# Kernel optimization log

Measured on AMD Instinct MI355X. Metric: run time of the kernel, lower is better.

Reference implementation:

```python
import jax, jax.numpy as jnp
import numpy as np

F = 512    # x_features
M = 8      # mid_features
C = 20     # classnum
B = 2048   # batch
MF = M * F

def _lin(k, fin, fout):
    k1, k2 = jax.random.split(k)
    s = 1.0 / np.sqrt(fin)
    W = jax.random.uniform(k1, (fout, fin), minval=-s, maxval=s, dtype=jnp.float32)
    b = jax.random.uniform(k2, (fout,), minval=-s, maxval=s, dtype=jnp.float32)
    return W, b

def setup_inputs():
    key = jax.random.key(0)
    ks = jax.random.split(key, 12)
    W1, b1 = _lin(ks[0], F, F)
    W2, b2 = _lin(ks[1], F, F)
    W3, b3 = _lin(ks[2], F, MF)
    W4, b4 = _lin(ks[3], F, MF)
    W5, b5 = _lin(ks[4], MF, C)
    W7, b7 = _lin(ks[5], MF, MF)
    W8, b8 = _lin(ks[6], MF, MF)
    W9, b9 = _lin(ks[7], MF, MF)
    x = jax.random.normal(ks[8], (B, F), dtype=jnp.float32)
    batch_label = jax.random.randint(ks[9], (B,), 0, C, dtype=jnp.int32)
    hs_init = jax.random.uniform(ks[10], (C, MF), dtype=jnp.float32)
    labels_init = jnp.zeros((C, MF), dtype=jnp.float32)
    return dict(x=x, batch_label=batch_label, W1=W1, b1=b1, W2=W2, b2=b2,
                W3=W3, b3=b3, W4=W4, b4=b4, W5=W5, b5=b5, W7=W7, b7=b7,
                W8=W8, b8=b8, W9=W9, b9=b9, hs_init=hs_init, labels_init=labels_init)

def reference(x, batch_label, W1, b1, W2, b2, W3, b3, W4, b4, W5, b5,
              W7, b7, W8, b8, W9, b9, hs_init, labels_init):
    h = jax.nn.relu(x @ W1.T + b1)
    h = jax.nn.relu(h @ W2.T + b2)
    label0 = jnp.tanh(h @ W3.T + b3)   # [B, MF]  (self.label_0)
    out = jnp.tanh(h @ W4.T + b4)      # [B, MF]
    gram = label0 @ label0.T           # [B, B]
    masks = batch_label[None, :] == jnp.arange(C, dtype=batch_label.dtype)[:, None]  # [C, B]
    counts = masks.sum(axis=1)         # [C]

    def attn_for_class(mask):
        # masked self-attention restricted to rows/cols of this class
        logits = jnp.where(mask[None, :], gram, -1e30)
        A = jax.nn.softmax(logits, axis=1)           # [B, B]
        attn = A @ label0                            # [B, MF]
        return jnp.sum(attn * mask[:, None].astype(attn.dtype), axis=0) / jnp.maximum(mask.sum(), 1)

    attn_labels = jax.vmap(attn_for_class)(masks)    # [C, MF]
    hs_new = jax.nn.sigmoid(attn_labels @ W7.T + b7 + hs_init @ W8.T + b8)
    hs_new = jax.lax.stop_gradient(hs_new)           # matches hs[i].detach_()
    nonempty = (counts > 0)[:, None]
    hs = jnp.where(nonempty, hs_new, hs_init)
    labels = jnp.where(nonempty, jnp.tanh(hs @ W9.T + b9), labels_init)  # [C, MF]
    # cosine similarity (torch eps = 1e-8)
    denom = jnp.maximum(jnp.linalg.norm(out, axis=1)[:, None] *
                        jnp.linalg.norm(labels, axis=1)[None, :], 1e-8)
    outs = (out @ labels.T) / denom                  # [B, C]  == outs.transpose(1,0)
    ls = jnp.tanh(labels @ W5.T + b5)                # [C, C]
    return jnp.concatenate([outs, ls], axis=0)       # [B+C, C]
```

## Files before the change

kernel.cpp:

```cpp
#include <hip/hip_runtime.h>
#include <hip/hip_bf16.h>
#include <math.h>

#define FDIM 512
#define MFD  4096
#define CNUM 20
#define BATCH 2048
#define SMAX 256
#define GKS  16
#define GBK  64
#define SKS  4
#define AJS  4

typedef __attribute__((ext_vector_type(8))) short bf16x8;
typedef __attribute__((ext_vector_type(4))) float f32x4;

__device__ inline unsigned short f2bf1(float f) {
  union { float f; unsigned u; } a; a.f = f;
  unsigned r = a.u + 0x7fffu + ((a.u >> 16) & 1u);
  return (unsigned short)(r >> 16);
}
__device__ inline float bf2f(unsigned short u) {
  union { unsigned u; float f; } a; a.u = ((unsigned)u) << 16; return a.f;
}
__device__ inline float fast_tanh(float x) {
  float cx = fminf(fmaxf(x, -15.f), 15.f);
  float e = __expf(2.f * cx);
  return (e - 1.f) / (e + 1.f);
}
__device__ inline float dot4acc(float4 a, float4 b, float acc) {
  acc = fmaf(a.x, b.x, acc); acc = fmaf(a.y, b.y, acc);
  acc = fmaf(a.z, b.z, acc); acc = fmaf(a.w, b.w, acc);
  return acc;
}
__device__ inline void gload_lds16(const void* g, void* l) {
  __builtin_amdgcn_global_load_lds(
      (const __attribute__((address_space(1))) unsigned int*)g,
      (__attribute__((address_space(3))) unsigned int*)l, 16, 0, 0);
}

__global__ __launch_bounds__(256) void cvt_bf16(const float* __restrict__ in,
                                                unsigned short* __restrict__ out, int n4) {
  int i = blockIdx.x * 256 + threadIdx.x;
  if (i >= n4) return;
  float4 v = ((const float4*)in)[i];
  ((ushort4*)out)[i] = make_ushort4(f2bf1(v.x), f2bf1(v.y), f2bf1(v.z), f2bf1(v.w));
}

template<int ACT, int OUTBF>
__global__ __launch_bounds__(256) void mfma_gemm(const unsigned short* __restrict__ A,
                                                 const unsigned short* __restrict__ B,
                                                 const float* __restrict__ bias,
                                                 float* __restrict__ Cf,
                                                 unsigned short* __restrict__ Cb,
                                                 int M, int N, int K) {
  __shared__ __align__(16) char lds[16384];
  const int t = threadIdx.x, lane = t & 63, w = t >> 6;
  const int wr = w >> 1, wc = w & 1;
  const int m0 = blockIdx.y * 128, n0 = blockIdx.x * 128;

  f32x4 acc[4][4];
#pragma unroll
  for (int m = 0; m < 4; ++m)
#pragma unroll
    for (int n = 0; n < 4; ++n) acc[m][n] = (f32x4){0.f, 0.f, 0.f, 0.f};

  int rS[2], qS[2];
#pragma unroll
  for (int i = 0; i < 2; ++i) {
    int t16 = (w * 2 + i) * 64 + lane;
    rS[i] = t16 >> 2;
    qS[i] = (t16 & 3) ^ ((rS[i] >> 1) & 3);
  }

  for (int k0 = 0; k0 < K; k0 += 32) {
#pragma unroll
    for (int i = 0; i < 2; ++i) {
      gload_lds16(A + (size_t)(m0 + rS[i]) * K + k0 + qS[i] * 8,
                  lds + (w * 2 + i) * 1024);
      gload_lds16(B + (size_t)(n0 + rS[i]) * K + k0 + qS[i] * 8,
                  lds + 8192 + (w * 2 + i) * 1024);
    }
    __syncthreads();

    bf16x8 af[4], bfr[4];
    const int kq = lane >> 4, l15 = lane & 15;
#pragma unroll
    for (int m = 0; m < 4; ++m) {
      int ra = wr * 64 + m * 16 + l15;
      af[m] = *(const bf16x8*)(lds + ra * 64 + ((kq ^ ((ra >> 1) & 3)) << 4));
      int rb = wc * 64 + m * 16 + l15;
      bfr[m] = *(const bf16x8*)(lds + 8192 + rb * 64 + ((kq ^ ((rb >> 1) & 3)) << 4));
    }
#pragma unroll
    for (int m = 0; m < 4; ++m)
#pragma unroll
      for (int n = 0; n < 4; ++n)
        acc[m][n] = __builtin_amdgcn_mfma_f32_16x16x32_bf16(af[m], bfr[n], acc[m][n], 0, 0, 0);
    __syncthreads();
  }

#pragma unroll
  for (int n = 0; n < 4; ++n) {
    int col = n0 + wc * 64 + n * 16 + (lane & 15);
    float bv = bias[col];
#pragma unroll
    for (int m = 0; m < 4; ++m) {
      int rbase = m0 + wr * 64 + m * 16 + ((lane >> 4) << 2);
#pragma unroll
      for (int j = 0; j < 4; ++j) {
        float v = acc[m][n][j] + bv;
        if (ACT == 1) v = fmaxf(v, 0.f);
        if (ACT == 2) v = fast_tanh(v);
        if (OUTBF) Cb[(size_t)(rbase + j) * N + col] = f2bf1(v);
        else       Cf[(size_t)(rbase + j) * N + col] = v;
      }
    }
  }
}

__global__ void build_idx(const int* __restrict__ label, int* __restrict__ idx,
                          int* __restrict__ counts) {
  __shared__ int cnt[CNUM];
  int t = threadIdx.x;
  if (t < CNUM) cnt[t] = 0;
  __syncthreads();
  for (int b = t; b < BATCH; b += 256) {
    int c = label[b];
    int p = atomicAdd(&cnt[c], 1);
    idx[c * BATCH + p] = b;
  }
  __syncthreads();
  if (t < CNUM) counts[t] = cnt[t];
}

__global__ __launch_bounds__(256) void gram_mfma(const unsigned short* __restrict__ Gb,
                                                 const int* __restrict__ idx,
                                                 const int* __restrict__ counts,
                                                 float* __restrict__ S) {
  const int c = blockIdx.z, n = counts[c];
  const int tp = blockIdx.y, ti = tp >> 1, tj = tp & 1;
  const int i0 = ti * 128, j0 = tj * 128;
  if (i0 >= n || j0 >= n) return;
  const int* idc = idx + c * BATCH;
  __shared__ __align__(16) char lds[32768];
  const bool same = (ti == tj);
  char* ldsB = same ? lds : (lds + 16384);

  const int t = threadIdx.x, lane = t & 63, w = t >> 6;
  size_t offA[4], offB[4];
#pragma unroll
  for (int q = 0; q < 4; ++q) {
    int t16 = q * 256 + t;
    int r = t16 >> 3, p = t16 & 7;
    int ch = p ^ (r & 7);
    int ia = i0 + r, jb = j0 + r;
    offA[q] = (size_t)idc[ia < n ? ia : 0] * MFD + ch * 8;
    offB[q] = (size_t)idc[jb < n ? jb : 0] * MFD + ch * 8;
  }
  const int kbeg = blockIdx.x * (MFD / GKS);

  f32x4 acc[2][8];
#pragma unroll
  for (int fi = 0; fi < 2; ++fi)
#pragma unroll
    for (int fj = 0; fj < 8; ++fj) acc[fi][fj] = (f32x4){0.f, 0.f, 0.f, 0.f};

  const int l15 = lane & 15, kq = lane >> 4;
  for (int k0 = kbeg; k0 < kbeg + MFD / GKS; k0 += GBK) {
#pragma unroll
    for (int q = 0; q < 4; ++q) {
      gload_lds16(Gb + offA[q] + k0, lds + q * 4096 + w * 1024 + (lane << 4));
      if (!same)
        gload_lds16(Gb + offB[q] + k0, ldsB + q * 4096 + w * 1024 + (lane << 4));
    }
    __syncthreads();
#pragma unroll
    for (int kk = 0; kk < 2; ++kk) {
      bf16x8 a[2], b[8];
#pragma unroll
      for (int fi = 0; fi < 2; ++fi) {
        int r = w * 32 + fi * 16 + l15;
        int sl = (kk * 4 + kq) ^ (r & 7);
        a[fi] = *(const bf16x8*)(lds + r * 128 + sl * 16);
      }
#pragma unroll
      for (int fj = 0; fj < 8; ++fj) {
        int r = fj * 16 + l15;
        int sl = (kk * 4 + kq) ^ (r & 7);
        b[fj] = *(const bf16x8*)(ldsB + r * 128 + sl * 16);
      }
#pragma unroll
      for (int fi = 0; fi < 2; ++fi)
#pragma unroll
        for (int fj = 0; fj < 8; ++fj)
          acc[fi][fj] = __builtin_amdgcn_mfma_f32_16x16x32_bf16(a[fi], b[fj], acc[fi][fj], 0, 0, 0);
    }
    __syncthreads();
  }

  float* Sc = S + (size_t)c * SMAX * SMAX;
#pragma unroll
  for (int fi = 0; fi < 2; ++fi) {
    int ibase = i0 + w * 32 + fi * 16 + (lane >> 4) * 4;
#pragma unroll
    for (int fj = 0; fj < 8; ++fj) {
      int j = j0 + fj * 16 + l15;
#pragma unroll
      for (int jj = 0; jj < 4; ++jj)
        atomicAdd(&Sc[(size_t)(ibase + jj) * SMAX + j], acc[fi][fj][jj]);
    }
  }
}

__global__ __launch_bounds__(256) void softmax_w2(const float* __restrict__ S,
                                                  const int* __restrict__ counts,
                                                  float* __restrict__ W) {
  const int c = blockIdx.y;
  const int n = counts[c];
  __shared__ float wacc[4][SMAX];
  const int t = threadIdx.x, lane = t & 63, wid = t >> 6;
  for (int j = t; j < 4 * SMAX; j += 256) (&wacc[0][0])[j] = 0.f;
  __syncthreads();
  const float* Sc = S + (size_t)c * SMAX * SMAX;
  for (int i = blockIdx.x * 4 + wid; i < n; i += 32) {
    const float* row = Sc + (size_t)i * SMAX;
    float v[4];
    float m = -INFINITY;
#pragma unroll
    for (int q = 0; q < 4; ++q) {
      int j = lane + q * 64;
      v[q] = (j < n) ? row[j] : -INFINITY;
      m = fmaxf(m, v[q]);
    }
#pragma unroll
    for (int s = 32; s; s >>= 1) m = fmaxf(m, __shfl_xor(m, s));
    float e[4], sum = 0.f;
#pragma unroll
    for (int q = 0; q < 4; ++q) {
      int j = lane + q * 64;
      e[q] = (j < n) ? expf(v[q] - m) : 0.f;
      sum += e[q];
    }
#pragma unroll
    for (int s = 32; s; s >>= 1) sum += __shfl_xor(sum, s);
    float inv = 1.f / sum;
#pragma unroll
    for (int q = 0; q < 4; ++q) {
      int j = lane + q * 64;
      if (j < n) wacc[wid][j] += e[q] * inv;
    }
  }
  __syncthreads();
  for (int j = t; j < SMAX; j += 256) {
    float v = wacc[0][j] + wacc[1][j] + wacc[2][j] + wacc[3][j];
    if (v != 0.f) atomicAdd(&W[c * SMAX + j], v);
  }
}

__global__ __launch_bounds__(256) void attn_combine3(const unsigned short* __restrict__ Gb,
                                                     const int* __restrict__ idx,
                                                     const int* __restrict__ counts,
                                                     const float* __restrict__ W,
                                                     float* __restrict__ attn) {
  const int c = blockIdx.z, n = counts[c];
  const int col2 = blockIdx.x * 256 + threadIdx.x;
  const int j0 = (n * (int)blockIdx.y) / AJS;
  const int j1 = (n * ((int)blockIdx.y + 1)) / AJS;
  const int* idc = idx + c * BATCH;
  const float* Wc = W + c * SMAX;
  float a0 = 0.f, a1 = 0.f;
  for (int j = j0; j < j1; ++j) {
    float wj = Wc[j];
    ushort2 g = ((const ushort2*)(Gb + (size_t)idc[j] * MFD))[col2];
    a0 = fmaf(wj, bf2f(g.x), a0);
    a1 = fmaf(wj, bf2f(g.y), a1);
  }
  if (j1 > j0) {
    float inv = 1.f / (float)n;
    atomicAdd(&attn[(size_t)c * MFD + col2 * 2],     a0 * inv);
    atomicAdd(&attn[(size_t)c * MFD + col2 * 2 + 1], a1 * inv);
  }
}

template<int TWO>
__global__ __launch_bounds__(256) void skinny_acc(const float* __restrict__ Wa,
                                                  const float* __restrict__ Aa,
                                                  const float* __restrict__ Wb,
                                                  const float* __restrict__ Ab,
                                                  float* __restrict__ accbuf) {
  const int t = threadIdx.x, lane = t & 63, wid = t >> 6;
  const int o = blockIdx.x * 4 + wid;
  const int kb4 = blockIdx.y * (MFD / 4 / SKS);
  const float4* W4a = (const float4*)Wa + (size_t)o * (MFD / 4) + kb4;
  const float4* W4b = (const float4*)Wb + (size_t)o * (MFD / 4) + kb4;
  const float4* A4a = (const float4*)Aa + kb4;
  const float4* A4b = (const float4*)Ab + kb4;
  float acc[CNUM] = {};
#pragma unroll
  for (int i = 0; i < MFD / 4 / SKS / 64; ++i) {
    int k4 = i * 64 + lane;
    float4 wv = W4a[k4];
    float4 wv2;
    if (TWO) wv2 = W4b[k4];
#pragma unroll
    for (int c = 0; c < CNUM; ++c) {
      acc[c] = dot4acc(A4a[(size_t)c * (MFD / 4) + k4], wv, acc[c]);
      if (TWO) acc[c] = dot4acc(A4b[(size_t)c * (MFD / 4) + k4], wv2, acc[c]);
    }
  }
#pragma unroll
  for (int c = 0; c < CNUM; ++c)
#pragma unroll
    for (int s = 32; s; s >>= 1) acc[c] += __shfl_xor(acc[c], s);
#pragma unroll
  for (int c = 0; c < CNUM; ++c)
    if (lane == c) atomicAdd(&accbuf[(size_t)o * CNUM + c], acc[c]);
}

__global__ __launch_bounds__(256) void finalize_hs(const float* __restrict__ accbuf,
                                                   const float* __restrict__ b7,
                                                   const float* __restrict__ b8,
                                                   const int* __restrict__ counts,
                                                   const float* __restrict__ hsin,
                                                   float* __restrict__ hs) {
  const int o = blockIdx.x * 256 + threadIdx.x;
  const float bb = b7[o] + b8[o];
#pragma unroll
  for (int c = 0; c < CNUM; ++c) {
    float v = accbuf[(size_t)o * CNUM + c] + bb;
    v = 1.f / (1.f + __expf(-v));
    hs[(size_t)c * MFD + o] = (counts[c] > 0) ? v : hsin[(size_t)c * MFD + o];
  }
}

__global__ __launch_bounds__(256) void finalize_lab(const float* __restrict__ accbuf,
                                                    const float* __restrict__ b9,
                                                    const int* __restrict__ counts,
                                                    const float* __restrict__ labinit,
                                                    float* __restrict__ labels) {
  const int o = blockIdx.x * 256 + threadIdx.x;
  const float bb = b9[o];
#pragma unroll
  for (int c = 0; c < CNUM; ++c) {
    float v = tanhf(accbuf[(size_t)o * CNUM + c] + bb);
    labels[(size_t)c * MFD + o] = (counts[c] > 0) ? v : labinit[(size_t)c * MFD + o];
  }
}

__global__ __launch_bounds__(256) void rownorm(const float* __restrict__ X,
                                               float* __restrict__ out, int ncols) {
  const int b = blockIdx.x, t = threadIdx.x;
  const float4* X4 = (const float4*)(X + (size_t)b * ncols);
  float ss = 0.f;
  for (int i = t; i < ncols / 4; i += 256) {
    float4 v = X4[i];
    ss = dot4acc(v, v, ss);
  }
#pragma unroll
  for (int s = 32; s; s >>= 1) ss += __shfl_xor(ss, s);
  __shared__ float red[4];
  const int lane = t & 63, wid = t >> 6;
  if (lane == 0) red[wid] = ss;
  __syncthreads();
  if (t == 0) out[b] = sqrtf(red[0] + red[1] + red[2] + red[3]);
}

__global__ __launch_bounds__(256) void outs_fused(const float* __restrict__ outb,
                                                  const float* __restrict__ labels,
                                                  const float* __restrict__ nl,
                                                  float* __restrict__ dout) {
  const int b = blockIdx.x, t = threadIdx.x;
  const float4* O4 = (const float4*)(outb + (size_t)b * MFD);
  const float4* L4 = (const float4*)labels;
  float acc[CNUM] = {};
  float ss = 0.f;
  for (int i = t; i < MFD / 4; i += 256) {
    float4 ov = O4[i];
    ss = dot4acc(ov, ov, ss);
#pragma unroll
    for (int c = 0; c < CNUM; ++c)
      acc[c] = dot4acc(ov, L4[(size_t)c * (MFD / 4) + i], acc[c]);
  }
#pragma unroll
  for (int s = 32; s; s >>= 1) ss += __shfl_xor(ss, s);
#pragma unroll
  for (int c = 0; c < CNUM; ++c)
#pragma unroll
    for (int s = 32; s; s >>= 1) acc[c] += __shfl_xor(acc[c], s);
  __shared__ float red[4][CNUM + 1];
  const int lane = t & 63, wid = t >> 6;
  if (lane == 0) {
#pragma unroll
    for (int c = 0; c < CNUM; ++c) red[wid][c] = acc[c];
    red[wid][CNUM] = ss;
  }
  __syncthreads();
  if (t < CNUM) {
    float v = red[0][t] + red[1][t] + red[2][t] + red[3][t];
    float nrm = sqrtf(red[0][CNUM] + red[1][CNUM] + red[2][CNUM] + red[3][CNUM]);
    float d = fmaxf(nrm * nl[t], 1e-8f);
    dout[(size_t)b * CNUM + t] = v / d;
  }
}

__global__ __launch_bounds__(256) void ls_kernel(const float* __restrict__ labels,
                                                 const float* __restrict__ W5,
                                                 const float* __restrict__ b5,
                                                 float* __restrict__ dout) {
  const int c1 = blockIdx.x, t = threadIdx.x;
  __shared__ float lrow[MFD];
  for (int i = t; i < MFD; i += 256) lrow[i] = labels[(size_t)c1 * MFD + i];
  __syncthreads();
  const int lane = t & 63, wid = t >> 6;
  for (int c2 = wid; c2 < CNUM; c2 += 4) {
    const float4* w = (const float4*)(W5 + (size_t)c2 * MFD);
    float acc = 0.f;
    for (int i = lane; i < MFD / 4; i += 64)
      acc = dot4acc(*(const float4*)&lrow[i * 4], w[i], acc);
#pragma unroll
    for (int s = 32; s; s >>= 1) acc += __shfl_xor(acc, s);
    if (lane == 0)
      dout[(size_t)(BATCH + c1) * CNUM + c2] = tanhf(acc + b5[c2]);
  }
}

extern "C" void kernel_launch(void* const* d_in, const int* in_sizes, int n_in,
                              void* d_out, int out_size, void* d_ws, size_t ws_size,
                              hipStream_t stream) {
  const float* x    = (const float*)d_in[0];
  const int*   lab  = (const int*)d_in[1];
  const float* W1 = (const float*)d_in[2];  const float* b1 = (const float*)d_in[3];
  const float* W2 = (const float*)d_in[4];  const float* b2 = (const float*)d_in[5];
  const float* W3 = (const float*)d_in[6];  const float* b3 = (const float*)d_in[7];
  const float* W4 = (const float*)d_in[8];  const float* b4 = (const float*)d_in[9];
  const float* W5 = (const float*)d_in[10]; const float* b5 = (const float*)d_in[11];
  const float* W7 = (const float*)d_in[12]; const float* b7 = (const float*)d_in[13];
  const float* W8 = (const float*)d_in[14]; const float* b8 = (const float*)d_in[15];
  const float* W9 = (const float*)d_in[16]; const float* b9 = (const float*)d_in[17];
  const float* hs_init  = (const float*)d_in[18];
  const float* lab_init = (const float*)d_in[19];
  float* out = (float*)d_out;

  char* base = (char*)d_ws;
  size_t off = 0;
  auto alloc = [&](size_t bytes) { char* p = base + off; off += (bytes + 255) & ~(size_t)255; return p; };

  unsigned short* xb  = (unsigned short*)alloc((size_t)BATCH * FDIM * 2);
  unsigned short* h1b = (unsigned short*)alloc((size_t)BATCH * FDIM * 2);
  unsigned short* h2b = (unsigned short*)alloc((size_t)BATCH * FDIM * 2);
  unsigned short* W1b = (unsigned short*)alloc((size_t)FDIM * FDIM * 2);
  unsigned short* W2b = (unsigned short*)alloc((size_t)FDIM * FDIM * 2);
  unsigned short* W3b = (unsigned short*)alloc((size_t)MFD * FDIM * 2);
  unsigned short* W4b = (unsigned short*)alloc((size_t)MFD * FDIM * 2);
  unsigned short* label0b = (unsigned short*)alloc((size_t)BATCH * MFD * 2);
  float* outb   = (float*)alloc((size_t)BATCH * MFD * 4);
  float* S      = (float*)alloc((size_t)CNUM * SMAX * SMAX * 4);
  float* wsum   = (float*)alloc((size_t)CNUM * SMAX * 4);
  float* attn   = (float*)alloc((size_t)CNUM * MFD * 4);
  float* accA   = (float*)alloc((size_t)MFD * CNUM * 4);
  float* accB   = (float*)alloc((size_t)MFD * CNUM * 4);
  float* hsbuf  = (float*)alloc((size_t)CNUM * MFD * 4);
  float* labels = (float*)alloc((size_t)CNUM * MFD * 4);
  float* nl     = (float*)alloc(64 * 4);
  int* idx      = (int*)alloc((size_t)CNUM * BATCH * 4);
  int* counts   = (int*)alloc(64 * 4);

  cvt_bf16<<<(BATCH * FDIM / 4 + 255) / 256, 256, 0, stream>>>(x,  xb,  BATCH * FDIM / 4);
  cvt_bf16<<<(FDIM * FDIM / 4 + 255) / 256, 256, 0, stream>>>(W1, W1b, FDIM * FDIM / 4);
  cvt_bf16<<<(FDIM * FDIM / 4 + 255) / 256, 256, 0, stream>>>(W2, W2b, FDIM * FDIM / 4);
  cvt_bf16<<<(MFD * FDIM / 4 + 255) / 256, 256, 0, stream>>>(W3, W3b, MFD * FDIM / 4);
  cvt_bf16<<<(MFD * FDIM / 4 + 255) / 256, 256, 0, stream>>>(W4, W4b, MFD * FDIM / 4);

  mfma_gemm<1, 1><<<dim3(FDIM / 128, BATCH / 128), 256, 0, stream>>>(xb,  W1b, b1, nullptr, h1b, BATCH, FDIM, FDIM);
  mfma_gemm<1, 1><<<dim3(FDIM / 128, BATCH / 128), 256, 0, stream>>>(h1b, W2b, b2, nullptr, h2b, BATCH, FDIM, FDIM);
  mfma_gemm<2, 1><<<dim3(MFD / 128, BATCH / 128), 256, 0, stream>>>(h2b, W3b, b3, nullptr, label0b, BATCH, MFD, FDIM);
  mfma_gemm<2, 0><<<dim3(MFD / 128, BATCH / 128), 256, 0, stream>>>(h2b, W4b, b4, outb,   nullptr,  BATCH, MFD, FDIM);

  build_idx<<<1, 256, 0, stream>>>(lab, idx, counts);
  hipMemsetAsync(S, 0, (size_t)CNUM * SMAX * SMAX * 4 + (size_t)CNUM * SMAX * 4 + (size_t)CNUM * MFD * 4, stream);
  hipMemsetAsync(accA, 0, (size_t)MFD * CNUM * 8, stream);
  gram_mfma<<<dim3(GKS, 4, CNUM), 256, 0, stream>>>(label0b, idx, counts, S);
  softmax_w2<<<dim3(8, CNUM), 256, 0, stream>>>(S, counts, wsum);
  attn_combine3<<<dim3(MFD / 512, AJS, CNUM), 256, 0, stream>>>(label0b, idx, counts, wsum, attn);

  skinny_acc<1><<<dim3(MFD / 4, SKS), 256, 0, stream>>>(W7, attn, W8, hs_init, accA);
  finalize_hs<<<MFD / 256, 256, 0, stream>>>(accA, b7, b8, counts, hs_init, hsbuf);
  skinny_acc<0><<<dim3(MFD / 4, SKS), 256, 0, stream>>>(W9, hsbuf, nullptr, nullptr, accB);
  finalize_lab<<<MFD / 256, 256, 0, stream>>>(accB, b9, counts, lab_init, labels);

  rownorm<<<CNUM, 256, 0, stream>>>(labels, nl, MFD);
  outs_fused<<<BATCH, 256, 0, stream>>>(outb, labels, nl, out);
  ls_kernel<<<CNUM, 256, 0, stream>>>(labels, W5, b5, out);
}
```

Measured before the change: 627.3 us.

## Stage skinny GEMV activations in LDS, compute four outputs per wave, merge conversions

Rewrites the skinny weight-times-class-matrix kernels so each block stages 20-row activation chunks in shared memory and each wave computes four output rows. The activation data is then read once per block instead of once per wave from global or L2. The five bf16 conversion launches are also merged into one kernel. The cost is more registers (80 accumulators), block-level synchronisation, and fewer blocks in the grid.

```diff
diff --git a/kernel.cpp b/kernel.cpp
--- a/kernel.cpp
+++ b/kernel.cpp
@@ -9,7 +9,7 @@
 #define SMAX 256
 #define GKS  16
 #define GBK  64
-#define SKS  4
+#define SKS2 4
 #define AJS  4
 
 typedef __attribute__((ext_vector_type(8))) short bf16x8;
@@ -39,12 +39,28 @@
       (__attribute__((address_space(3))) unsigned int*)l, 16, 0, 0);
 }
 
-__global__ __launch_bounds__(256) void cvt_bf16(const float* __restrict__ in,
-                                                unsigned short* __restrict__ out, int n4) {
+__global__ __launch_bounds__(256) void cvt_all(const float* __restrict__ x,
+                                               const float* __restrict__ W1,
+                                               const float* __restrict__ W2,
+                                               const float* __restrict__ W3,
+                                               const float* __restrict__ W4,
+                                               unsigned short* __restrict__ xb,
+                                               unsigned short* __restrict__ W1b,
+                                               unsigned short* __restrict__ W2b,
+                                               unsigned short* __restrict__ W3b,
+                                               unsigned short* __restrict__ W4b) {
+  const int N0 = BATCH * FDIM / 4;
+  const int NW = FDIM * FDIM / 4;
+  const int NB = MFD * FDIM / 4;
   int i = blockIdx.x * 256 + threadIdx.x;
-  if (i >= n4) return;
-  float4 v = ((const float4*)in)[i];
-  ((ushort4*)out)[i] = make_ushort4(f2bf1(v.x), f2bf1(v.y), f2bf1(v.z), f2bf1(v.w));
+  const float* src; unsigned short* dst; int j;
+  if (i < N0)                    { src = x;  dst = xb;  j = i; }
+  else if (i < N0 + NW)          { src = W1; dst = W1b; j = i - N0; }
+  else if (i < N0 + 2 * NW)      { src = W2; dst = W2b; j = i - N0 - NW; }
+  else if (i < N0 + 2 * NW + NB) { src = W3; dst = W3b; j = i - N0 - 2 * NW; }
+  else                           { src = W4; dst = W4b; j = i - N0 - 2 * NW - NB; }
+  float4 v = ((const float4*)src)[j];
+  ((ushort4*)dst)[j] = make_ushort4(f2bf1(v.x), f2bf1(v.y), f2bf1(v.z), f2bf1(v.w));
 }
 
 template<int ACT, int OUTBF>
@@ -284,38 +300,59 @@
 }
 
 template<int TWO>
-__global__ __launch_bounds__(256) void skinny_acc(const float* __restrict__ Wa,
+__global__ __launch_bounds__(256) void skinny_lds(const float* __restrict__ Wa,
                                                   const float* __restrict__ Aa,
                                                   const float* __restrict__ Wb,
                                                   const float* __restrict__ Ab,
                                                   float* __restrict__ accbuf) {
+  __shared__ float As[(TWO ? 2 : 1) * CNUM][256];
   const int t = threadIdx.x, lane = t & 63, wid = t >> 6;
-  const int o = blockIdx.x * 4 + wid;
-  const int kb4 = blockIdx.y * (MFD / 4 / SKS);
-  const float4* W4a = (const float4*)Wa + (size_t)o * (MFD / 4) + kb4;
-  const float4* W4b = (const float4*)Wb + (size_t)o * (MFD / 4) + kb4;
-  const float4* A4a = (const float4*)Aa + kb4;
-  const float4* A4b = (const float4*)Ab + kb4;
-  float acc[CNUM] = {};
-#pragma unroll
-  for (int i = 0; i < MFD / 4 / SKS / 64; ++i) {
-    int k4 = i * 64 + lane;
-    float4 wv = W4a[k4];
-    float4 wv2;
-    if (TWO) wv2 = W4b[k4];
+  const int o0 = blockIdx.x * 16 + wid * 4;
+  const int NM = TWO ? 2 : 1;
+  float acc[CNUM][4] = {};
+  for (int ph = 0; ph < 4; ++ph) {
+    const int kb = blockIdx.y * (MFD / SKS2) + ph * 256;
+    for (int i = t; i < NM * CNUM * 64; i += 256) {
+      int m = i / (CNUM * 64);
+      int rem = i - m * (CNUM * 64);
+      int c = rem >> 6, k4 = rem & 63;
+      const float* src = m ? Ab : Aa;
+      *(float4*)&As[m * CNUM + c][k4 * 4] =
+          *((const float4*)(src + (size_t)c * MFD + kb) + k4);
+    }
+    __syncthreads();
+    float4 wva[4], wvb[4];
+#pragma unroll
+    for (int oo = 0; oo < 4; ++oo) {
+      wva[oo] = *((const float4*)(Wa + (size_t)(o0 + oo) * MFD + kb) + lane);
+      if (TWO) wvb[oo] = *((const float4*)(Wb + (size_t)(o0 + oo) * MFD + kb) + lane);
+    }
 #pragma unroll
     for (int c = 0; c < CNUM; ++c) {
-      acc[c] = dot4acc(A4a[(size_t)c * (MFD / 4) + k4], wv, acc[c]);
-      if (TWO) acc[c] = dot4acc(A4b[(size_t)c * (MFD / 4) + k4], wv2, acc[c]);
-    }
+      float4 av = *((const float4*)As[c] + lane);
+#pragma unroll
+      for (int oo = 0; oo < 4; ++oo) acc[c][oo] = dot4acc(av, wva[oo], acc[c][oo]);
+      if (TWO) {
+        float4 bv = *((const float4*)As[CNUM + c] + lane);
+#pragma unroll
+        for (int oo = 0; oo < 4; ++oo) acc[c][oo] = dot4acc(bv, wvb[oo], acc[c][oo]);
+      }
+    }
+    __syncthreads();
   }
 #pragma unroll
   for (int c = 0; c < CNUM; ++c)
 #pragma unroll
-    for (int s = 32; s; s >>= 1) acc[c] += __shfl_xor(acc[c], s);
+    for (int oo = 0; oo < 4; ++oo)
+#pragma unroll
+      for (int s = 32; s; s >>= 1) acc[c][oo] += __shfl_xor(acc[c][oo], s);
 #pragma unroll
   for (int c = 0; c < CNUM; ++c)
-    if (lane == c) atomicAdd(&accbuf[(size_t)o * CNUM + c], acc[c]);
+    if (lane == c) {
+#pragma unroll
+      for (int oo = 0; oo < 4; ++oo)
+        atomicAdd(&accbuf[(size_t)(o0 + oo) * CNUM + c], acc[c][oo]);
+    }
 }
 
 __global__ __launch_bounds__(256) void finalize_hs(const float* __restrict__ accbuf,
@@ -466,11 +503,10 @@
   int* idx      = (int*)alloc((size_t)CNUM * BATCH * 4);
   int* counts   = (int*)alloc(64 * 4);
 
-  cvt_bf16<<<(BATCH * FDIM / 4 + 255) / 256, 256, 0, stream>>>(x,  xb,  BATCH * FDIM / 4);
-  cvt_bf16<<<(FDIM * FDIM / 4 + 255) / 256, 256, 0, stream>>>(W1, W1b, FDIM * FDIM / 4);
-  cvt_bf16<<<(FDIM * FDIM / 4 + 255) / 256, 256, 0, stream>>>(W2, W2b, FDIM * FDIM / 4);
-  cvt_bf16<<<(MFD * FDIM / 4 + 255) / 256, 256, 0, stream>>>(W3, W3b, MFD * FDIM / 4);
-  cvt_bf16<<<(MFD * FDIM / 4 + 255) / 256, 256, 0, stream>>>(W4, W4b, MFD * FDIM / 4);
+  {
+    const int total4 = BATCH * FDIM / 4 + 2 * (FDIM * FDIM / 4) + 2 * (MFD * FDIM / 4);
+    cvt_all<<<total4 / 256, 256, 0, stream>>>(x, W1, W2, W3, W4, xb, W1b, W2b, W3b, W4b);
+  }
 
   mfma_gemm<1, 1><<<dim3(FDIM / 128, BATCH / 128), 256, 0, stream>>>(xb,  W1b, b1, nullptr, h1b, BATCH, FDIM, FDIM);
   mfma_gemm<1, 1><<<dim3(FDIM / 128, BATCH / 128), 256, 0, stream>>>(h1b, W2b, b2, nullptr, h2b, BATCH, FDIM, FDIM);
@@ -484,9 +520,9 @@
   softmax_w2<<<dim3(8, CNUM), 256, 0, stream>>>(S, counts, wsum);
   attn_combine3<<<dim3(MFD / 512, AJS, CNUM), 256, 0, stream>>>(label0b, idx, counts, wsum, attn);
 
-  skinny_acc<1><<<dim3(MFD / 4, SKS), 256, 0, stream>>>(W7, attn, W8, hs_init, accA);
+  skinny_lds<1><<<dim3(MFD / 16, SKS2), 256, 0, stream>>>(W7, attn, W8, hs_init, accA);
   finalize_hs<<<MFD / 256, 256, 0, stream>>>(accA, b7, b8, counts, hs_init, hsbuf);
-  skinny_acc<0><<<dim3(MFD / 4, SKS), 256, 0, stream>>>(W9, hsbuf, nullptr, nullptr, accB);
+  skinny_lds<0><<<dim3(MFD / 16, SKS2), 256, 0, stream>>>(W9, hsbuf, nullptr, nullptr, accB);
   finalize_lab<<<MFD / 256, 256, 0, stream>>>(accB, b9, counts, lab_init, labels);
 
   rownorm<<<CNUM, 256, 0, stream>>>(labels, nl, MFD);
```

Result: faster. 513.6 us (-18.1%).
